# Performance work log

Hardware: AMD Instinct MI355X
Metric: run time of the kernel (lower is better)

The kernel has to match this reference:

```python
import jax, jax.numpy as jnp
import numpy as np

B, N, D, H = 128, 512, 128, 8
DH = D // H
CLIP = 10.0          # tanh_clipping
NEG = -1.0e9         # finite -inf for masking (keeps grads clean)


def setup_inputs() -> dict:
    key = jax.random.key(0)
    ks = jax.random.split(key, 6)
    s = 0.08  # ~1/sqrt(D) init scale so pre-tanh logits are in a sane range
    return {
        "embeddings": jax.random.normal(ks[0], (B, N, D), jnp.float32),
        "W_node_proj": jax.random.normal(ks[1], (D, 3 * D), jnp.float32) * s,
        "W_fixed_ctx": jax.random.normal(ks[2], (D, D), jnp.float32) * s,
        "W_step_ctx": jax.random.normal(ks[3], (2 * D, D), jnp.float32) * s,
        "W_out": jax.random.normal(ks[4], (D, D), jnp.float32) * s,
        "W_placeholder": jax.random.uniform(ks[5], (2 * D,), jnp.float32, -1.0, 1.0),
    }


def reference(embeddings, W_node_proj, W_fixed_ctx, W_step_ctx, W_out, W_placeholder):
    # _precompute: fixed context + glimpse K/V + logit key (cached for all steps)
    graph_embed = embeddings.mean(axis=1)                    # [B,D]
    fixed_ctx = graph_embed @ W_fixed_ctx                    # [B,D]
    proj = embeddings @ W_node_proj                          # [B,N,3D]
    gK, gV, logit_K = jnp.split(proj, 3, axis=-1)
    gK = gK.reshape(B, N, H, DH)                             # glimpse key heads
    gV = gV.reshape(B, N, H, DH)                             # glimpse val heads
    inv_sqrt_dh = 1.0 / jnp.sqrt(jnp.float32(DH))
    inv_sqrt_d = 1.0 / jnp.sqrt(jnp.float32(D))
    batch_idx = jnp.arange(B)

    def step(carry, _):
        visited, first, prev, i = carry
        # step context: placeholder at i==0, else concat(first, current) embeddings
        cur_ctx = jnp.concatenate(
            [embeddings[batch_idx, first], embeddings[batch_idx, prev]], axis=-1)  # [B,2D]
        step_ctx = jnp.where(i == 0, W_placeholder[None, :], cur_ctx)
        q = fixed_ctx + step_ctx @ W_step_ctx                # [B,D]
        qh = q.reshape(B, H, DH)
        # masked multi-head glimpse attention
        compat = jnp.einsum('bhd,bnhd->bhn', qh, gK) * inv_sqrt_dh
        compat = jnp.where(visited[:, None, :], NEG, compat)
        attn = jax.nn.softmax(compat, axis=-1)
        heads = jnp.einsum('bhn,bnhd->bhd', attn, gV)
        glimpse = heads.reshape(B, D) @ W_out                # project_out
        # logit attention with tanh clipping
        logits = jnp.einsum('bd,bnd->bn', glimpse, logit_K) * inv_sqrt_d
        logits = CLIP * jnp.tanh(logits)
        logits = jnp.where(visited, NEG, logits)
        log_p = jax.nn.log_softmax(logits, axis=-1)
        sel = jnp.argmax(log_p, axis=-1).astype(jnp.int32)   # greedy decode
        visited = visited.at[batch_idx, sel].set(True)
        first = jnp.where(i == 0, sel, first)
        return (visited, first, sel, i + 1), (log_p, sel)

    init = (jnp.zeros((B, N), bool), jnp.zeros((B,), jnp.int32),
            jnp.zeros((B,), jnp.int32), jnp.int32(0))
    _, (log_ps, pis) = jax.lax.scan(step, init, None, length=N)
    log_p = jnp.transpose(log_ps, (1, 0, 2))                 # [B,N_steps,N]
    pi = jnp.transpose(pis, (1, 0))                          # [B,N_steps]
    # _calc_log_likelihood
    ll = jnp.take_along_axis(log_p, pi[:, :, None], axis=2).squeeze(-1).sum(axis=1)
    return log_p, pi, ll
```

## Files before the change

### kernel.cpp

```cpp
#include <hip/hip_runtime.h>
#include <hip/hip_bf16.h>
#include <math.h>

#define BATCH 128
#define NN 512
#define DD 128
#define D3 384
#define NEGV (-1.0e9f)
#define NEGINF (-1.0e30f)

__global__ __launch_bounds__(256) void k_fixed(const float* __restrict__ emb,
                                               const float* __restrict__ Wf,
                                               const float* __restrict__ Wstep,
                                               const float* __restrict__ Wph,
                                               float* __restrict__ fixedc,
                                               float* __restrict__ q0) {
  const int b = blockIdx.x;
  __shared__ float s_part[2][DD];
  __shared__ float s_ge[DD];
  const int tid = threadIdx.x;
  const int d = tid & 127, c = tid >> 7;
  const float* e = emb + (size_t)b * NN * DD;
  float acc = 0.f;
  for (int n = c * 256; n < c * 256 + 256; ++n) acc += e[(size_t)n * DD + d];
  s_part[c][d] = acc;
  __syncthreads();
  if (tid < DD) s_ge[tid] = (s_part[0][tid] + s_part[1][tid]) * (1.0f / 512.0f);
  __syncthreads();
  if (tid < DD) {
    float a = 0.f;
    for (int k = 0; k < DD; ++k) a += s_ge[k] * Wf[k * DD + tid];
    fixedc[b * DD + tid] = a;
    float pq = 0.f;
    for (int k = 0; k < 2 * DD; ++k) pq += Wph[k] * Wstep[k * DD + tid];
    q0[b * DD + tid] = a + pq;
  }
}

__global__ __launch_bounds__(384) void k_proj(const float* __restrict__ emb,
                                              const float* __restrict__ Wp,
                                              float* __restrict__ proj) {
  const size_t row0 = (size_t)blockIdx.x * 32;
  __shared__ float s_A[32][DD];
  const int tid = threadIdx.x;
  for (int t = tid; t < 32 * DD; t += 384)
    s_A[t >> 7][t & 127] = emb[row0 * DD + t];
  __syncthreads();
  float acc[32];
#pragma unroll
  for (int r = 0; r < 32; ++r) acc[r] = 0.f;
  const int c = tid;
  for (int k = 0; k < DD; ++k) {
    float w = Wp[k * D3 + c];
#pragma unroll
    for (int r = 0; r < 32; ++r) acc[r] += s_A[r][k] * w;
  }
  for (int r = 0; r < 32; ++r) proj[(row0 + r) * D3 + c] = acc[r];
}

__global__ __launch_bounds__(128) void k_lp(float* __restrict__ proj,
                                            const float* __restrict__ Wout) {
  const size_t row0 = (size_t)blockIdx.x * 32;
  __shared__ float s_L[32][DD];
  const int tid = threadIdx.x;
  for (int rr = 0; rr < 32; ++rr)
    s_L[rr][tid] = proj[(row0 + rr) * D3 + 2 * DD + tid];
  __syncthreads();
  float acc[32];
#pragma unroll
  for (int r = 0; r < 32; ++r) acc[r] = 0.f;
  for (int d = 0; d < DD; ++d) {
    const float w = Wout[tid * DD + d];
#pragma unroll
    for (int r = 0; r < 32; ++r) acc[r] += w * s_L[r][d];
  }
  for (int r = 0; r < 32; ++r)
    proj[(row0 + r) * D3 + 2 * DD + tid] = acc[r];
}

__global__ __launch_bounds__(256) void k_ectx(const float* __restrict__ emb,
                                              const float* __restrict__ Wstep,
                                              const float* __restrict__ fixedc,
                                              float* __restrict__ E12) {
  const size_t row0 = (size_t)blockIdx.x * 32;
  __shared__ float s_A[32][DD];
  const int tid = threadIdx.x;
  for (int t = tid; t < 32 * DD; t += 256)
    s_A[t >> 7][t & 127] = emb[row0 * DD + t];
  __syncthreads();
  float acc[32];
#pragma unroll
  for (int r = 0; r < 32; ++r) acc[r] = 0.f;
  const int c = tid;
  const int b = (int)(row0 >> 9);
  const float* wp = (c < DD) ? (Wstep + c) : (Wstep + DD * DD + (c - DD));
  for (int k = 0; k < DD; ++k) {
    float w = wp[(size_t)k * DD];
#pragma unroll
    for (int r = 0; r < 32; ++r) acc[r] += s_A[r][k] * w;
  }
  const float fc = (c < DD) ? fixedc[b * DD + c] : 0.f;
  for (int r = 0; r < 32; ++r) E12[(row0 + r) * 256 + c] = acc[r] + fc;
}

#define DOT16(q, F)                                                           \
  (q[0] * F[0].x + q[1] * F[0].y + q[2] * F[0].z + q[3] * F[0].w +            \
   q[4] * F[1].x + q[5] * F[1].y + q[6] * F[1].z + q[7] * F[1].w +            \
   q[8] * F[2].x + q[9] * F[2].y + q[10] * F[2].z + q[11] * F[2].w +          \
   q[12] * F[3].x + q[13] * F[3].y + q[14] * F[3].z + q[15] * F[3].w)

#define L_LOAD(njx, Lr)                                                       \
  {                                                                           \
    const float4* lp_ =                                                       \
        (const float4*)(projb + (size_t)(njx)*D3 + 2 * DD + h * 16);          \
    Lr[0] = lp_[0]; Lr[1] = lp_[1]; Lr[2] = lp_[2]; Lr[3] = lp_[3];           \
  }

#define L_CONSUME(Lr, njx, LGR)                                               \
  {                                                                           \
    float a_ = DOT16(gf, Lr);                                                 \
    a_ += __shfl_xor(a_, 1);                                                  \
    a_ += __shfl_xor(a_, 2);                                                  \
    a_ += __shfl_xor(a_, 4);                                                  \
    if (h == 0) {                                                             \
      LGR = 10.0f * tanhf(a_ * inv_sqrt_d);                                   \
      asum += expf(LGR);                                                      \
      if (LGR > av || (LGR == av && (njx) < ai)) { av = LGR; ai = (njx); }    \
    }                                                                         \
  }

__device__ __forceinline__ void barrier_rlx() {
  asm volatile("s_waitcnt lgkmcnt(0)" ::: "memory");
  __builtin_amdgcn_s_barrier();
  asm volatile("" ::: "memory");
}

__global__ __launch_bounds__(1024, 1) void k_decode(
    const float* __restrict__ emb, const float* __restrict__ proj,
    const float* __restrict__ fixedc, const float* __restrict__ q0,
    const float* __restrict__ E12, const float* __restrict__ Wstep,
    const float* __restrict__ Wph, const int useE, float* __restrict__ out) {
  const int b = blockIdx.x;
  const int tid = threadIdx.x;
  const int lane = tid & 63;
  const int wave = tid >> 6;
  const int h = tid & 7, r = tid >> 3;

  __shared__ float4 s_Lpf[2][4][16][64];
  __shared__ int s_idx[NN];
  __shared__ int s_pos[NN];
  __shared__ unsigned char s_visited[NN];
  __shared__ float s_hacc[16][8][17];
  __shared__ float s_heads[DD];
  __shared__ float s_rm[16];
  __shared__ int s_ri[16];
  __shared__ float s_es[16];
  __shared__ float s_q[DD];
  __shared__ float s_ctx[2 * DD];
  __shared__ int s_first, s_prev, s_M, s_swap;
  __shared__ float s_ll, s_lzv;

  const float inv_sqrt_d = 0.08838834764831845f;
  const size_t eb = (size_t)b * NN * DD;
  const size_t e2 = (size_t)b * NN * 256;
  const float* projb = proj + (size_t)b * NN * D3;
  float* outp = out + (size_t)b * NN * NN;
  const size_t PI_OFF = (size_t)BATCH * NN * NN;
  const size_t LL_OFF = PI_OFF + (size_t)BATCH * NN;

  if (tid < NN) {
    s_idx[tid] = tid;
    s_pos[tid] = tid;
    s_visited[tid] = 0;
  }
  if (tid == 0) { s_first = 0; s_prev = 0; s_ll = 0.f; s_M = NN; }
#pragma unroll
  for (int s = 0; s < 2; ++s) {
    const float4* lp =
        (const float4*)(projb + (size_t)(r + s * 128) * D3 + 2 * DD + h * 16);
    s_Lpf[s][0][wave][lane] = lp[0];
    s_Lpf[s][1][wave][lane] = lp[1];
    s_Lpf[s][2][wave][lane] = lp[2];
    s_Lpf[s][3][wave][lane] = lp[3];
  }
  __syncthreads();

  for (int i = 0; i < NN; ++i) {
    const int M = s_M;
    const int first = s_first, prev = s_prev;

    float qf[16];
    if (useE) {
      if (i == 0) {
#pragma unroll
        for (int d = 0; d < 4; ++d) {
          const float4 v = *(const float4*)(q0 + b * DD + h * 16 + d * 4);
          qf[d * 4 + 0] = v.x; qf[d * 4 + 1] = v.y;
          qf[d * 4 + 2] = v.z; qf[d * 4 + 3] = v.w;
        }
      } else {
        const float* e1p = E12 + e2 + (size_t)first * 256 + h * 16;
        const float* e2p = E12 + e2 + (size_t)prev * 256 + DD + h * 16;
#pragma unroll
        for (int d = 0; d < 4; ++d) {
          const float4 a = *(const float4*)(e1p + d * 4);
          const float4 c = *(const float4*)(e2p + d * 4);
          qf[d * 4 + 0] = a.x + c.x;
          qf[d * 4 + 1] = a.y + c.y;
          qf[d * 4 + 2] = a.z + c.z;
          qf[d * 4 + 3] = a.w + c.w;
        }
      }
    } else {
      if (tid < 2 * DD) {
        float v;
        if (i == 0)
          v = Wph[tid];
        else
          v = (tid < DD) ? emb[eb + (size_t)first * DD + tid]
                         : emb[eb + (size_t)prev * DD + (tid - DD)];
        s_ctx[tid] = v;
      }
      __syncthreads();
      if (tid < DD) {
        float a = fixedc[b * DD + tid];
        for (int k = 0; k < 2 * DD; ++k) a += s_ctx[k] * Wstep[k * DD + tid];
        s_q[tid] = a;
      }
      __syncthreads();
#pragma unroll
      for (int d = 0; d < 16; ++d) qf[d] = s_q[h * 16 + d];
    }

    bool act[4];
    int nj[4];
#pragma unroll
    for (int k = 0; k < 4; ++k) {
      const int j = r + k * 128;
      act[k] = (j < M);
      nj[k] = s_idx[j];
    }
    float s_l = 0.f;
    float acc[16];
#pragma unroll
    for (int d = 0; d < 16; ++d) acc[d] = 0.f;
#pragma unroll
    for (int k = 0; k < 4; ++k) {
      if (act[k]) {
        const float* rp = projb + (size_t)nj[k] * D3 + h * 16;
        const float4* kp = (const float4*)rp;
        float4 k0 = kp[0], k1 = kp[1], k2 = kp[2], k3 = kp[3];
        float a = qf[0] * k0.x + qf[1] * k0.y + qf[2] * k0.z + qf[3] * k0.w +
                  qf[4] * k1.x + qf[5] * k1.y + qf[6] * k1.z + qf[7] * k1.w +
                  qf[8] * k2.x + qf[9] * k2.y + qf[10] * k2.z + qf[11] * k2.w +
                  qf[12] * k3.x + qf[13] * k3.y + qf[14] * k3.z +
                  qf[15] * k3.w;
        const float p = expf(a * 0.25f);
        s_l += p;
        const float4* vp = (const float4*)(rp + DD);
        float4 v0 = vp[0], v1 = vp[1], v2 = vp[2], v3 = vp[3];
        acc[0] += p * v0.x;  acc[1] += p * v0.y;
        acc[2] += p * v0.z;  acc[3] += p * v0.w;
        acc[4] += p * v1.x;  acc[5] += p * v1.y;
        acc[6] += p * v1.z;  acc[7] += p * v1.w;
        acc[8] += p * v2.x;  acc[9] += p * v2.y;
        acc[10] += p * v2.z; acc[11] += p * v2.w;
        acc[12] += p * v3.x; acc[13] += p * v3.y;
        acc[14] += p * v3.z; acc[15] += p * v3.w;
      }
    }
    {
      const bool k1 = (lane & 8) == 0;
#pragma unroll
      for (int d = 0; d < 8; ++d) {
        const float send = k1 ? acc[d + 8] : acc[d];
        const float got = __shfl_xor(send, 8);
        acc[d] = (k1 ? acc[d] : acc[d + 8]) + got;
      }
      const bool k2 = (lane & 16) == 0;
#pragma unroll
      for (int d = 0; d < 4; ++d) {
        const float send = k2 ? acc[d + 4] : acc[d];
        const float got = __shfl_xor(send, 16);
        acc[d] = (k2 ? acc[d] : acc[d + 4]) + got;
      }
      const bool k3 = (lane & 32) == 0;
#pragma unroll
      for (int d = 0; d < 2; ++d) {
        const float send = k3 ? acc[d + 2] : acc[d];
        const float got = __shfl_xor(send, 32);
        acc[d] = (k3 ? acc[d] : acc[d + 2]) + got;
      }
    }
    s_l += __shfl_xor(s_l, 8);
    s_l += __shfl_xor(s_l, 16);
    s_l += __shfl_xor(s_l, 32);
    {
      const int dim0 = ((lane & 8) ? 8 : 0) | ((lane & 16) ? 4 : 0) |
                       ((lane & 32) ? 2 : 0);
      s_hacc[wave][h][dim0] = acc[0];
      s_hacc[wave][h][dim0 + 1] = acc[1];
      if (lane < 8) s_hacc[wave][lane][16] = s_l;
    }
    float4 Lf2[4], Lf3[4];
    {
      const int j2 = r + 256, j3 = r + 384;
      const int nj2p = s_idx[(j2 < M) ? j2 : (M - 1)];
      const int nj3p = s_idx[(j3 < M) ? j3 : (M - 1)];
      L_LOAD(nj2p, Lf2);
      L_LOAD(nj3p, Lf3);
    }
    barrier_rlx();

    if (tid < DD) {
      const int hh = tid >> 4, dh = tid & 15;
      float num = 0.f, den = 0.f;
#pragma unroll
      for (int w = 0; w < 16; ++w) {
        num += s_hacc[w][hh][dh];
        den += s_hacc[w][hh][16];
      }
      s_heads[tid] = num / den;
    }
    barrier_rlx();

    float gf[16];
#pragma unroll
    for (int d = 0; d < 16; ++d) gf[d] = s_heads[h * 16 + d];
    float av = NEGINF;
    int ai = 0x7FFFFFFF;
    float asum = 0.f;
    float lgr0 = 0.f, lgr1 = 0.f, lgr2 = 0.f, lgr3 = 0.f;
    if (act[0]) {
      float4 LA[4];
      LA[0] = s_Lpf[0][0][wave][lane];
      LA[1] = s_Lpf[0][1][wave][lane];
      LA[2] = s_Lpf[0][2][wave][lane];
      LA[3] = s_Lpf[0][3][wave][lane];
      L_CONSUME(LA, nj[0], lgr0);
    }
    if (act[1]) {
      float4 LA[4];
      LA[0] = s_Lpf[1][0][wave][lane];
      LA[1] = s_Lpf[1][1][wave][lane];
      LA[2] = s_Lpf[1][2][wave][lane];
      LA[3] = s_Lpf[1][3][wave][lane];
      L_CONSUME(LA, nj[1], lgr1);
    }
    if (act[2]) { L_CONSUME(Lf2, nj[2], lgr2); }
    if (act[3]) { L_CONSUME(Lf3, nj[3], lgr3); }
    const int visn = (tid < NN) ? (int)s_visited[tid] : 0;
#pragma unroll
    for (int off = 1; off <= 32; off <<= 1) {
      const float ov = __shfl_xor(av, off);
      const int oi = __shfl_xor(ai, off);
      asum += __shfl_xor(asum, off);
      if (ov > av || (ov == av && oi < ai)) { av = ov; ai = oi; }
    }
    if (lane == 0) { s_rm[wave] = av; s_ri[wave] = ai; s_es[wave] = asum; }
    barrier_rlx();

    if (wave == 0) {
      float cv = (lane < 16) ? s_rm[lane] : NEGINF;
      int ci = (lane < 16) ? s_ri[lane] : 0x7FFFFFFF;
      float cs = (lane < 16) ? s_es[lane] : 0.f;
#pragma unroll
      for (int off = 1; off <= 8; off <<= 1) {
        const float ov = __shfl_xor(cv, off);
        const int oi = __shfl_xor(ci, off);
        cs += __shfl_xor(cs, off);
        if (ov > cv || (ov == cv && oi < ci)) { cv = ov; ci = oi; }
      }
      if (lane == 0) {
        const float lzv = logf(cs);
        const int sel = ci;
        s_lzv = lzv;
        s_ll += cv - lzv;
        s_visited[sel] = 1;
        if (i == 0) s_first = sel;
        s_prev = sel;
        out[PI_OFF + (size_t)b * NN + i] = (float)sel;
        const int p = s_pos[sel];
        const int last = s_idx[M - 1];
        s_idx[p] = last;
        s_pos[last] = p;
        s_idx[M - 1] = sel;
        s_pos[sel] = M - 1;
        s_M = M - 1;
        s_swap = p;
      }
    }
    barrier_rlx();

    {
      const int sp = s_swap;
      if (sp < 256 && r == (sp & 127)) {
        const int sl = sp >> 7;
        const int nr = s_idx[sp];
        const float4* lp =
            (const float4*)(projb + (size_t)nr * D3 + 2 * DD + h * 16);
        s_Lpf[sl][0][wave][lane] = lp[0];
        s_Lpf[sl][1][wave][lane] = lp[1];
        s_Lpf[sl][2][wave][lane] = lp[2];
        s_Lpf[sl][3][wave][lane] = lp[3];
      }
    }
    const float lz = s_lzv;
    if (h == 0) {
      if (act[0]) outp[(size_t)i * NN + nj[0]] = lgr0 - lz;
      if (act[1]) outp[(size_t)i * NN + nj[1]] = lgr1 - lz;
      if (act[2]) outp[(size_t)i * NN + nj[2]] = lgr2 - lz;
      if (act[3]) outp[(size_t)i * NN + nj[3]] = lgr3 - lz;
    }
    if (tid < NN && visn) outp[(size_t)i * NN + tid] = NEGV - lz;
  }
  if (tid == 0) out[LL_OFF + b] = s_ll;
}

extern "C" void kernel_launch(void* const* d_in, const int* in_sizes, int n_in,
                              void* d_out, int out_size, void* d_ws,
                              size_t ws_size, hipStream_t stream) {
  const float* emb = (const float*)d_in[0];
  const float* Wnp = (const float*)d_in[1];
  const float* Wf = (const float*)d_in[2];
  const float* Wstep = (const float*)d_in[3];
  const float* Wout = (const float*)d_in[4];
  const float* Wph = (const float*)d_in[5];
  float* out = (float*)d_out;

  const size_t projN = (size_t)BATCH * NN * D3;
  const size_t eN = (size_t)BATCH * NN * 256;
  const size_t need_full = (projN + eN + 2 * (size_t)BATCH * DD) * 4;

  float* proj = (float*)d_ws;
  float* E12 = proj + projN;
  const int useE = (ws_size >= need_full) ? 1 : 0;
  float* fixedc = useE ? (E12 + eN) : (proj + projN);
  float* q0 = fixedc + (size_t)BATCH * DD;

  k_fixed<<<BATCH, 256, 0, stream>>>(emb, Wf, Wstep, Wph, fixedc, q0);
  k_proj<<<(BATCH * NN) / 32, 384, 0, stream>>>(emb, Wnp, proj);
  k_lp<<<(BATCH * NN) / 32, 128, 0, stream>>>(proj, Wout);
  if (useE) k_ectx<<<(BATCH * NN) / 32, 256, 0, stream>>>(emb, Wstep, fixedc, E12);
  k_decode<<<BATCH, 1024, 0, stream>>>(emb, proj, fixedc, q0,
                                       useE ? E12 : nullptr, Wstep, Wph, useE,
                                       out);
}
```

Before: 5.842 ms.

## Halve decode block to 512 threads with 8 nodes per thread and staged logits

```diff
diff --git a/kernel.cpp b/kernel.cpp
--- a/kernel.cpp
+++ b/kernel.cpp
@@ -109,33 +109,13 @@
    q[8] * F[2].x + q[9] * F[2].y + q[10] * F[2].z + q[11] * F[2].w +          \
    q[12] * F[3].x + q[13] * F[3].y + q[14] * F[3].z + q[15] * F[3].w)
 
-#define L_LOAD(njx, Lr)                                                       \
-  {                                                                           \
-    const float4* lp_ =                                                       \
-        (const float4*)(projb + (size_t)(njx)*D3 + 2 * DD + h * 16);          \
-    Lr[0] = lp_[0]; Lr[1] = lp_[1]; Lr[2] = lp_[2]; Lr[3] = lp_[3];           \
-  }
-
-#define L_CONSUME(Lr, njx, LGR)                                               \
-  {                                                                           \
-    float a_ = DOT16(gf, Lr);                                                 \
-    a_ += __shfl_xor(a_, 1);                                                  \
-    a_ += __shfl_xor(a_, 2);                                                  \
-    a_ += __shfl_xor(a_, 4);                                                  \
-    if (h == 0) {                                                             \
-      LGR = 10.0f * tanhf(a_ * inv_sqrt_d);                                   \
-      asum += expf(LGR);                                                      \
-      if (LGR > av || (LGR == av && (njx) < ai)) { av = LGR; ai = (njx); }    \
-    }                                                                         \
-  }
-
 __device__ __forceinline__ void barrier_rlx() {
   asm volatile("s_waitcnt lgkmcnt(0)" ::: "memory");
   __builtin_amdgcn_s_barrier();
   asm volatile("" ::: "memory");
 }
 
-__global__ __launch_bounds__(1024, 1) void k_decode(
+__global__ __launch_bounds__(512, 1) void k_decode(
     const float* __restrict__ emb, const float* __restrict__ proj,
     const float* __restrict__ fixedc, const float* __restrict__ q0,
     const float* __restrict__ E12, const float* __restrict__ Wstep,
@@ -146,15 +126,16 @@
   const int wave = tid >> 6;
   const int h = tid & 7, r = tid >> 3;
 
-  __shared__ float4 s_Lpf[2][4][16][64];
+  __shared__ float4 s_Lpf[4][4][512];
   __shared__ int s_idx[NN];
   __shared__ int s_pos[NN];
   __shared__ unsigned char s_visited[NN];
-  __shared__ float s_hacc[16][8][17];
+  __shared__ float s_hacc[8][8][17];
   __shared__ float s_heads[DD];
-  __shared__ float s_rm[16];
-  __shared__ int s_ri[16];
-  __shared__ float s_es[16];
+  __shared__ float s_logits[NN];
+  __shared__ float s_rm[8];
+  __shared__ int s_ri[8];
+  __shared__ float s_es[8];
   __shared__ float s_q[DD];
   __shared__ float s_ctx[2 * DD];
   __shared__ int s_first, s_prev, s_M, s_swap;
@@ -168,20 +149,18 @@
   const size_t PI_OFF = (size_t)BATCH * NN * NN;
   const size_t LL_OFF = PI_OFF + (size_t)BATCH * NN;
 
-  if (tid < NN) {
-    s_idx[tid] = tid;
-    s_pos[tid] = tid;
-    s_visited[tid] = 0;
-  }
+  s_idx[tid] = tid;
+  s_pos[tid] = tid;
+  s_visited[tid] = 0;
   if (tid == 0) { s_first = 0; s_prev = 0; s_ll = 0.f; s_M = NN; }
 #pragma unroll
-  for (int s = 0; s < 2; ++s) {
+  for (int k = 0; k < 4; ++k) {
     const float4* lp =
-        (const float4*)(projb + (size_t)(r + s * 128) * D3 + 2 * DD + h * 16);
-    s_Lpf[s][0][wave][lane] = lp[0];
-    s_Lpf[s][1][wave][lane] = lp[1];
-    s_Lpf[s][2][wave][lane] = lp[2];
-    s_Lpf[s][3][wave][lane] = lp[3];
+        (const float4*)(projb + (size_t)(r + 64 * k) * D3 + 2 * DD + h * 16);
+    s_Lpf[k][0][tid] = lp[0];
+    s_Lpf[k][1][tid] = lp[1];
+    s_Lpf[k][2][tid] = lp[2];
+    s_Lpf[k][3][tid] = lp[3];
   }
   __syncthreads();
 
@@ -232,43 +211,56 @@
       for (int d = 0; d < 16; ++d) qf[d] = s_q[h * 16 + d];
     }
 
-    bool act[4];
-    int nj[4];
-#pragma unroll
-    for (int k = 0; k < 4; ++k) {
-      const int j = r + k * 128;
+    bool act[8];
+    int nj[8];
+#pragma unroll
+    for (int k = 0; k < 8; ++k) {
+      const int j = r + 64 * k;
       act[k] = (j < M);
       nj[k] = s_idx[j];
     }
+
     float s_l = 0.f;
     float acc[16];
 #pragma unroll
     for (int d = 0; d < 16; ++d) acc[d] = 0.f;
-#pragma unroll
-    for (int k = 0; k < 4; ++k) {
-      if (act[k]) {
-        const float* rp = projb + (size_t)nj[k] * D3 + h * 16;
-        const float4* kp = (const float4*)rp;
-        float4 k0 = kp[0], k1 = kp[1], k2 = kp[2], k3 = kp[3];
-        float a = qf[0] * k0.x + qf[1] * k0.y + qf[2] * k0.z + qf[3] * k0.w +
-                  qf[4] * k1.x + qf[5] * k1.y + qf[6] * k1.z + qf[7] * k1.w +
-                  qf[8] * k2.x + qf[9] * k2.y + qf[10] * k2.z + qf[11] * k2.w +
-                  qf[12] * k3.x + qf[13] * k3.y + qf[14] * k3.z +
-                  qf[15] * k3.w;
-        const float p = expf(a * 0.25f);
-        s_l += p;
-        const float4* vp = (const float4*)(rp + DD);
-        float4 v0 = vp[0], v1 = vp[1], v2 = vp[2], v3 = vp[3];
-        acc[0] += p * v0.x;  acc[1] += p * v0.y;
-        acc[2] += p * v0.z;  acc[3] += p * v0.w;
-        acc[4] += p * v1.x;  acc[5] += p * v1.y;
-        acc[6] += p * v1.z;  acc[7] += p * v1.w;
-        acc[8] += p * v2.x;  acc[9] += p * v2.y;
-        acc[10] += p * v2.z; acc[11] += p * v2.w;
-        acc[12] += p * v3.x; acc[13] += p * v3.y;
-        acc[14] += p * v3.z; acc[15] += p * v3.w;
-      }
-    }
+
+#define KV_GROUP(K0)                                                          \
+    {                                                                         \
+      float4 Kf[4][4], Vf[4][4];                                              \
+      _Pragma("unroll")                                                       \
+      for (int k = 0; k < 4; ++k) {                                           \
+        if (act[K0 + k]) {                                                    \
+          const float* rp = projb + (size_t)nj[K0 + k] * D3 + h * 16;         \
+          const float4* kp = (const float4*)rp;                               \
+          Kf[k][0] = kp[0]; Kf[k][1] = kp[1];                                 \
+          Kf[k][2] = kp[2]; Kf[k][3] = kp[3];                                 \
+          const float4* vp = (const float4*)(rp + DD);                        \
+          Vf[k][0] = vp[0]; Vf[k][1] = vp[1];                                 \
+          Vf[k][2] = vp[2]; Vf[k][3] = vp[3];                                 \
+        }                                                                     \
+      }                                                                       \
+      _Pragma("unroll")                                                       \
+      for (int k = 0; k < 4; ++k) {                                           \
+        if (act[K0 + k]) {                                                    \
+          const float a = DOT16(qf, Kf[k]);                                   \
+          const float p = expf(a * 0.25f);                                    \
+          s_l += p;                                                           \
+          acc[0] += p * Vf[k][0].x;  acc[1] += p * Vf[k][0].y;                \
+          acc[2] += p * Vf[k][0].z;  acc[3] += p * Vf[k][0].w;                \
+          acc[4] += p * Vf[k][1].x;  acc[5] += p * Vf[k][1].y;                \
+          acc[6] += p * Vf[k][1].z;  acc[7] += p * Vf[k][1].w;                \
+          acc[8] += p * Vf[k][2].x;  acc[9] += p * Vf[k][2].y;                \
+          acc[10] += p * Vf[k][2].z; acc[11] += p * Vf[k][2].w;               \
+          acc[12] += p * Vf[k][3].x; acc[13] += p * Vf[k][3].y;               \
+          acc[14] += p * Vf[k][3].z; acc[15] += p * Vf[k][3].w;               \
+        }                                                                     \
+      }                                                                       \
+    }
+
+    KV_GROUP(0);
+    if (M > 256) KV_GROUP(4);
+
     {
       const bool k1 = (lane & 8) == 0;
 #pragma unroll
@@ -302,13 +294,17 @@
       s_hacc[wave][h][dim0 + 1] = acc[1];
       if (lane < 8) s_hacc[wave][lane][16] = s_l;
     }
-    float4 Lf2[4], Lf3[4];
-    {
-      const int j2 = r + 256, j3 = r + 384;
-      const int nj2p = s_idx[(j2 < M) ? j2 : (M - 1)];
-      const int nj3p = s_idx[(j3 < M) ? j3 : (M - 1)];
-      L_LOAD(nj2p, Lf2);
-      L_LOAD(nj3p, Lf3);
+    float4 Lf[4][4];
+    if (M > 256) {
+#pragma unroll
+      for (int k = 0; k < 4; ++k) {
+        if (act[4 + k]) {
+          const float4* lp =
+              (const float4*)(projb + (size_t)nj[4 + k] * D3 + 2 * DD + h * 16);
+          Lf[k][0] = lp[0]; Lf[k][1] = lp[1];
+          Lf[k][2] = lp[2]; Lf[k][3] = lp[3];
+        }
+      }
     }
     barrier_rlx();
 
@@ -316,40 +312,55 @@
       const int hh = tid >> 4, dh = tid & 15;
       float num = 0.f, den = 0.f;
 #pragma unroll
-      for (int w = 0; w < 16; ++w) {
+      for (int w = 0; w < 8; ++w) {
         num += s_hacc[w][hh][dh];
         den += s_hacc[w][hh][16];
       }
       s_heads[tid] = num / den;
     }
+    if (s_visited[tid]) s_logits[tid] = NEGV;
     barrier_rlx();
 
     float gf[16];
 #pragma unroll
     for (int d = 0; d < 16; ++d) gf[d] = s_heads[h * 16 + d];
+    float aa[8];
+#pragma unroll
+    for (int k = 0; k < 4; ++k) {
+      if (act[k]) {
+        float4 LA[4];
+        LA[0] = s_Lpf[k][0][tid];
+        LA[1] = s_Lpf[k][1][tid];
+        LA[2] = s_Lpf[k][2][tid];
+        LA[3] = s_Lpf[k][3][tid];
+        aa[k] = DOT16(gf, LA);
+      }
+    }
+    if (M > 256) {
+#pragma unroll
+      for (int k = 0; k < 4; ++k)
+        if (act[4 + k]) aa[4 + k] = DOT16(gf, Lf[k]);
+    }
+#pragma unroll
+    for (int off = 1; off <= 4; off <<= 1) {
+#pragma unroll
+      for (int k = 0; k < 8; ++k)
+        if (act[k]) aa[k] += __shfl_xor(aa[k], off);
+    }
     float av = NEGINF;
     int ai = 0x7FFFFFFF;
     float asum = 0.f;
-    float lgr0 = 0.f, lgr1 = 0.f, lgr2 = 0.f, lgr3 = 0.f;
-    if (act[0]) {
-      float4 LA[4];
-      LA[0] = s_Lpf[0][0][wave][lane];
-      LA[1] = s_Lpf[0][1][wave][lane];
-      LA[2] = s_Lpf[0][2][wave][lane];
-      LA[3] = s_Lpf[0][3][wave][lane];
-      L_CONSUME(LA, nj[0], lgr0);
-    }
-    if (act[1]) {
-      float4 LA[4];
-      LA[0] = s_Lpf[1][0][wave][lane];
-      LA[1] = s_Lpf[1][1][wave][lane];
-      LA[2] = s_Lpf[1][2][wave][lane];
-      LA[3] = s_Lpf[1][3][wave][lane];
-      L_CONSUME(LA, nj[1], lgr1);
-    }
-    if (act[2]) { L_CONSUME(Lf2, nj[2], lgr2); }
-    if (act[3]) { L_CONSUME(Lf3, nj[3], lgr3); }
-    const int visn = (tid < NN) ? (int)s_visited[tid] : 0;
+    if (h == 0) {
+#pragma unroll
+      for (int k = 0; k < 8; ++k) {
+        if (act[k]) {
+          const float lg = 10.0f * tanhf(aa[k] * inv_sqrt_d);
+          s_logits[nj[k]] = lg;
+          asum += expf(lg);
+          if (lg > av || (lg == av && nj[k] < ai)) { av = lg; ai = nj[k]; }
+        }
+      }
+    }
 #pragma unroll
     for (int off = 1; off <= 32; off <<= 1) {
       const float ov = __shfl_xor(av, off);
@@ -361,11 +372,11 @@
     barrier_rlx();
 
     if (wave == 0) {
-      float cv = (lane < 16) ? s_rm[lane] : NEGINF;
-      int ci = (lane < 16) ? s_ri[lane] : 0x7FFFFFFF;
-      float cs = (lane < 16) ? s_es[lane] : 0.f;
-#pragma unroll
-      for (int off = 1; off <= 8; off <<= 1) {
+      float cv = (lane < 8) ? s_rm[lane] : NEGINF;
+      int ci = (lane < 8) ? s_ri[lane] : 0x7FFFFFFF;
+      float cs = (lane < 8) ? s_es[lane] : 0.f;
+#pragma unroll
+      for (int off = 1; off <= 4; off <<= 1) {
         const float ov = __shfl_xor(cv, off);
         const int oi = __shfl_xor(ci, off);
         cs += __shfl_xor(cs, off);
@@ -394,25 +405,19 @@
 
     {
       const int sp = s_swap;
-      if (sp < 256 && r == (sp & 127)) {
-        const int sl = sp >> 7;
+      if (sp < 256 && r == (sp & 63)) {
+        const int sl = sp >> 6;
         const int nr = s_idx[sp];
         const float4* lp =
             (const float4*)(projb + (size_t)nr * D3 + 2 * DD + h * 16);
-        s_Lpf[sl][0][wave][lane] = lp[0];
-        s_Lpf[sl][1][wave][lane] = lp[1];
-        s_Lpf[sl][2][wave][lane] = lp[2];
-        s_Lpf[sl][3][wave][lane] = lp[3];
+        s_Lpf[sl][0][tid] = lp[0];
+        s_Lpf[sl][1][tid] = lp[1];
+        s_Lpf[sl][2][tid] = lp[2];
+        s_Lpf[sl][3][tid] = lp[3];
       }
     }
     const float lz = s_lzv;
-    if (h == 0) {
-      if (act[0]) outp[(size_t)i * NN + nj[0]] = lgr0 - lz;
-      if (act[1]) outp[(size_t)i * NN + nj[1]] = lgr1 - lz;
-      if (act[2]) outp[(size_t)i * NN + nj[2]] = lgr2 - lz;
-      if (act[3]) outp[(size_t)i * NN + nj[3]] = lgr3 - lz;
-    }
-    if (tid < NN && visn) outp[(size_t)i * NN + tid] = NEGV - lz;
+    outp[(size_t)i * NN + tid] = s_logits[tid] - lz;
   }
   if (tid == 0) out[LL_OFF + b] = s_ll;
 }
@@ -442,7 +447,7 @@
   k_proj<<<(BATCH * NN) / 32, 384, 0, stream>>>(emb, Wnp, proj);
   k_lp<<<(BATCH * NN) / 32, 128, 0, stream>>>(proj, Wout);
   if (useE) k_ectx<<<(BATCH * NN) / 32, 256, 0, stream>>>(emb, Wstep, fixedc, E12);
-  k_decode<<<BATCH, 1024, 0, stream>>>(emb, proj, fixedc, q0,
-                                       useE ? E12 : nullptr, Wstep, Wph, useE,
-                                       out);
-}
+  k_decode<<<BATCH, 512, 0, stream>>>(emb, proj, fixedc, q0,
+                                      useE ? E12 : nullptr, Wstep, Wph, useE,
+                                      out);
+}
```

Result: slower. 9.553 ms (+63.5%).
